# Performance work log

Measured on AMD Instinct MI355X. Metric: run time of the kernel, lower is better.

Reference implementation:

```python
import jax, jax.numpy as jnp
import numpy as np

N_AGENTS = 8
N_ENEMIES = 8
N_ALLIES = 7
H = 64            # rnn_hidden_dim (must be 64: Encoder latent dim hardcoded to 64, fed to fc3)
HEADS = 2         # hpn_head_num
OUT_NORMAL = 6    # output_normal_actions
N_ACTIONS = OUT_NORMAL + N_ENEMIES  # 14, required by expand_as in original code
E_DIM = 8
A_DIM = 8
OWN_DIM = 30
HYPER = 64        # hpn_hyper_dim
ENC_HID = 128     # predict_net_dim
BS = 2048


def _gru_cell(x, h, Wih, Whh, bih, bhh):
    # torch GRUCell math, gate order (r, z, n)
    gi = x @ Wih + bih
    gh = h @ Whh + bhh
    ir, iz, inn = jnp.split(gi, 3, axis=-1)
    hr, hz, hn = jnp.split(gh, 3, axis=-1)
    r = jax.nn.sigmoid(ir + hr)
    z = jax.nn.sigmoid(iz + hz)
    n = jnp.tanh(inn + r * hn)
    return (1.0 - z) * n + z * h


def setup_inputs() -> dict:
    key = jax.random.key(0)
    ks = jax.random.split(key, 48)
    B = BS * N_AGENTS

    def w(k, shape):
        return jax.random.normal(k, shape, dtype=jnp.float32) * 0.05

    he_out = ((E_DIM + 1) * H + 1) * HEADS   # 1154
    ha_out = A_DIM * H * HEADS               # 1024 (non-MMM map)

    return {
        "bs": BS,
        "own_feats": jax.random.normal(ks[0], (B, OWN_DIM), jnp.float32),
        "enemy_feats": jax.random.normal(ks[1], (B * N_ENEMIES, E_DIM), jnp.float32),
        "ally_feats": jax.random.normal(ks[2], (B * N_ALLIES, A_DIM), jnp.float32),
        "agent_ids": jax.random.randint(ks[3], (B,), 0, N_AGENTS),
        "last_action_ids": jax.random.randint(ks[4], (B,), 0, N_ACTIONS),
        "hidden_state": jax.random.normal(ks[5], (B, H), jnp.float32) * 0.1,
        "fc1_own_W": w(ks[6], (OWN_DIM, H)), "fc1_own_b": w(ks[7], (H,)),
        "agent_emb": w(ks[8], (N_AGENTS, H)),
        "action_emb": w(ks[9], (N_ACTIONS, H)),
        "he_W1": w(ks[10], (E_DIM, HYPER)), "he_b1": w(ks[11], (HYPER,)),
        "he_W2": w(ks[12], (HYPER, he_out)), "he_b2": w(ks[13], (he_out,)),
        "ha_W1": w(ks[14], (A_DIM, HYPER)), "ha_b1": w(ks[15], (HYPER,)),
        "ha_W2": w(ks[16], (HYPER, ha_out)), "ha_b2": w(ks[17], (ha_out,)),
        "merger_in_w": jnp.ones((1, HEADS, H), jnp.float32),
        "merger_out_w": jnp.ones((1, HEADS, 1), jnp.float32),
        "gru_Wih": w(ks[18], (H, 3 * H)), "gru_Whh": w(ks[19], (H, 3 * H)),
        "gru_bih": w(ks[20], (3 * H,)), "gru_bhh": w(ks[21], (3 * H,)),
        "fc2n_W": w(ks[22], (H, OUT_NORMAL)), "fc2n_b": w(ks[23], (OUT_NORMAL,)),
        "fc1b_W": w(ks[24], (OWN_DIM, H)), "fc1b_b": w(ks[25], (H,)),
        "gru2_Wih": w(ks[26], (H, 3 * H)), "gru2_Whh": w(ks[27], (H, 3 * H)),
        "gru2_bih": w(ks[28], (3 * H,)), "gru2_bhh": w(ks[29], (3 * H,)),
        "enc_W1": w(ks[30], (H, ENC_HID)), "enc_b1": w(ks[31], (ENC_HID,)),
        "enc_W2": w(ks[32], (ENC_HID, H)), "enc_b2": w(ks[33], (H,)),
        "fc3_W": w(ks[34], (H, N_ACTIONS)), "fc3_b": w(ks[35], (N_ACTIONS,)),
        "mlp_W": w(ks[36], (N_AGENTS, H, N_ACTIONS)), "mlp_b": w(ks[37], (N_AGENTS, N_ACTIONS)),
    }


def reference(bs, own_feats, enemy_feats, ally_feats, agent_ids, last_action_ids,
              hidden_state, fc1_own_W, fc1_own_b, agent_emb, action_emb,
              he_W1, he_b1, he_W2, he_b2, ha_W1, ha_b1, ha_W2, ha_b2,
              merger_in_w, merger_out_w, gru_Wih, gru_Whh, gru_bih, gru_bhh,
              fc2n_W, fc2n_b, fc1b_W, fc1b_b, gru2_Wih, gru2_Whh, gru2_bih, gru2_bhh,
              enc_W1, enc_b1, enc_W2, enc_b2, fc3_W, fc3_b, mlp_W, mlp_b):
    B = bs * N_AGENTS

    # own embedding + id/action embeddings
    emb_own = own_feats @ fc1_own_W + fc1_own_b
    emb_own = emb_own + agent_emb[agent_ids] + action_emb[last_action_ids]

    # hypernet-generated per-enemy fc1 weights, applied per entity, summed over enemies
    he = jax.nn.relu(enemy_feats @ he_W1 + he_b1) @ he_W2 + he_b2  # [B*E, 1154]
    cut = (H + 1) * HEADS
    w1e = he[:, :-cut].reshape(-1, E_DIM, H * HEADS)               # [B*E, e_dim, H*heads]
    emb_en = jnp.einsum('nd,ndk->nk', enemy_feats, w1e)
    emb_en = emb_en.reshape(B, N_ENEMIES, HEADS, H).sum(axis=1)    # [B, heads, H]

    ha = jax.nn.relu(ally_feats @ ha_W1 + ha_b1) @ ha_W2 + ha_b2   # [B*A, 1024]
    w1a = ha.reshape(-1, A_DIM, H * HEADS)
    emb_al = jnp.einsum('nd,ndk->nk', ally_feats, w1a)
    emb_al = emb_al.reshape(B, N_ALLIES, HEADS, H).sum(axis=1)     # [B, heads, H]

    # Merger over heads (softmax-weighted sum)
    mw = jax.nn.softmax(merger_in_w, axis=1)                       # [1, heads, H]
    merged = jnp.sum(mw * (emb_en + emb_al), axis=1)               # [B, H]

    x = jax.nn.relu(emb_own + merged)
    hh = _gru_cell(x, hidden_state, gru_Wih, gru_Whh, gru_bih, gru_bhh)  # [B, H]

    q_normal = (hh @ fc2n_W + fc2n_b).reshape(bs, N_AGENTS, OUT_NORMAL)

    # hypernet-generated attack output heads
    w2 = he[:, -cut:-HEADS].reshape(B, N_ENEMIES, H, HEADS)
    w2 = w2.transpose(0, 2, 1, 3).reshape(B, H, N_ENEMIES * HEADS)
    b2 = he[:, -HEADS:].reshape(B, N_ENEMIES * HEADS)
    qa = jnp.einsum('bh,bhk->bk', hh, w2) + b2                     # [B, E*heads]
    qa = qa.reshape(B * N_ENEMIES, HEADS)
    mo = jax.nn.softmax(merger_out_w[:, :, 0], axis=1)             # [1, heads]
    q_attack = jnp.sum(mo * qa, axis=1).reshape(bs, N_AGENTS, N_ENEMIES)

    q = jnp.concatenate([q_normal, q_attack], axis=-1)             # [bs, n_agents, 14]

    # parallel fc1 -> single-step GRU -> encoder branch
    x2 = jax.nn.relu(own_feats @ fc1b_W + fc1b_b)                  # [B, H]
    g = _gru_cell(x2, hidden_state, gru2_Wih, gru2_Whh, gru2_bih, gru2_bhh)  # [B, H]
    z = jax.nn.relu(g @ enc_W1 + enc_b1) @ enc_W2 + enc_b2         # [B, 64] encoder latent
    q_f = (z @ fc3_W + fc3_b).reshape(bs, N_AGENTS, N_ACTIONS)

    # per-agent mlps applied to first n_agents rows of gru output (as in original)
    ga = g[:N_AGENTS]                                              # [n_agents, H]
    local_q = jnp.einsum('ah,ahk->ak', ga, mlp_W) + mlp_b          # [n_agents, n_actions]
    local_qe = jnp.broadcast_to(local_q[None], q.shape)

    q_total = q + local_qe + q_f
    return (q_total, hh.reshape(bs, N_AGENTS, H), local_qe, q_f)
```

## Files before the change

kernel.cpp:

```cpp
#include <hip/hip_runtime.h>

#define HH_OFF 229376
#define LQE_OFF 1277952
#define QF_OFF 1507328

#define WS_HE 0
#define WS_HA 33280
#define WS_ATT 66560
#define WS_BATT 70656
#define WS_BH 70720
#define WS_BC 70784
#define WS_LQ 70800
#define WS_G1 70912
#define WS_G2 95488
#define WS_E1 120064
#define WS_E2 128256
#define WS_F1 136448
#define WS_END 140544

#define SSTR 640
#define BSTR 384

struct Params {
  const float *own, *ef, *af, *hid;
  const int *aid, *lid;
  const float *fc1oW, *fc1ob, *aemb, *actemb;
  const float *heW1, *heb1, *heW2, *heb2;
  const float *haW1, *hab1, *haW2, *hab2;
  const float *mi, *mo;
  const float *gWih, *gWhh, *gbih, *gbhh;
  const float *fc2nW, *fc2nb;
  const float *fc1bW, *fc1bb;
  const float *g2Wih, *g2Whh, *g2bih, *g2bhh;
  const float *eW1, *eb1, *eW2, *eb2;
  const float *fc3W, *fc3b;
  const float *mlpW, *mlpb;
};

__device__ __forceinline__ float sigm(float x) {
  x = fminf(fmaxf(x, -30.f), 30.f);
  return 1.f / (1.f + __expf(-x));
}
__device__ __forceinline__ float tanh_(float x) {
  x = fminf(fmaxf(x, -15.f), 15.f);
  float e = __expf(-2.f * x);
  return (1.f - e) / (1.f + e);
}

__global__ void __launch_bounds__(512) prep_kernel(Params p, float* __restrict__ ws) {
  const int tid = threadIdx.x;
  if (blockIdx.x == 0) {
    __shared__ float g8[8][64];
    __shared__ float x2s[8][64];
    const int w = __builtin_amdgcn_readfirstlane(tid >> 6);
    const int lane = tid & 63;
    {
      float acc = p.fc1bb[lane];
      const float* ow = p.own + w * 30;
      for (int d = 0; d < 30; ++d) acc += ow[d] * p.fc1bW[d * 64 + lane];
      x2s[w][lane] = fmaxf(acc, 0.f);
      float a0 = p.g2bih[lane], a1 = p.g2bih[64 + lane], a2 = p.g2bih[128 + lane];
      float b0 = p.g2bhh[lane], b1 = p.g2bhh[64 + lane], b2 = p.g2bhh[128 + lane];
      const float* hidw = p.hid + w * 64;
      for (int k = 0; k < 64; ++k) {
        float xk = x2s[w][k];
        float hk = hidw[k];
        a0 += xk * p.g2Wih[k * 192 + lane];
        a1 += xk * p.g2Wih[k * 192 + 64 + lane];
        a2 += xk * p.g2Wih[k * 192 + 128 + lane];
        b0 += hk * p.g2Whh[k * 192 + lane];
        b1 += hk * p.g2Whh[k * 192 + 64 + lane];
        b2 += hk * p.g2Whh[k * 192 + 128 + lane];
      }
      float r = sigm(a0 + b0), z = sigm(a1 + b1);
      float n = tanh_(a2 + r * b2);
      g8[w][lane] = (1.f - z) * n + z * hidw[lane];
    }
    __syncthreads();
    if (tid < 112) {
      int a = tid / 14, c = tid % 14;
      float lacc = p.mlpb[a * 14 + c];
      for (int h = 0; h < 64; ++h) lacc += g8[a][h] * p.mlpW[(a * 64 + h) * 14 + c];
      ws[WS_LQ + tid] = lacc;
    }
    return;
  }
  const int idx = (int)(blockIdx.x - 1) * 512 + tid;
  if (idx >= WS_END) return;
  const float mo0 = sigm(p.mo[0] - p.mo[1]);
  const float mo1 = 1.f - mo0;
  if (idx < 33280) {
    int c = idx >> 8, rem = idx & 255, h = rem >> 2, q = rem & 3;
    int t = c * 4 + q;
    float mw0 = sigm(p.mi[h] - p.mi[64 + h]);
    float mw1 = 1.f - mw0;
    float v;
    if (t < 512) {
      int d = t >> 6, j = t & 63;
      v = mw0 * p.heW2[j * 1154 + d * 128 + h] + mw1 * p.heW2[j * 1154 + d * 128 + 64 + h];
    } else {
      int d = t - 512;
      v = mw0 * p.heb2[d * 128 + h] + mw1 * p.heb2[d * 128 + 64 + h];
    }
    ws[WS_HE + idx] = v;
  } else if (idx < 66560) {
    int rel = idx - 33280;
    int c = rel >> 8, rem = rel & 255, h = rem >> 2, q = rem & 3;
    int t = c * 4 + q;
    float mw0 = sigm(p.mi[h] - p.mi[64 + h]);
    float mw1 = 1.f - mw0;
    float v;
    if (t < 512) {
      int d = t >> 6, j = t & 63;
      v = mw0 * p.haW2[j * 1024 + d * 128 + h] + mw1 * p.haW2[j * 1024 + d * 128 + 64 + h];
    } else {
      int d = t - 512;
      v = mw0 * p.hab2[d * 128 + h] + mw1 * p.hab2[d * 128 + 64 + h];
    }
    ws[WS_HA + rel] = v;
  } else if (idx < 70656) {
    int rel = idx - 66560;
    int c = rel >> 8, rem = rel & 255, j = rem >> 2, q = rem & 3;
    int h = c * 4 + q;
    ws[WS_ATT + rel] = mo0 * p.heW2[j * 1154 + 1024 + 2 * h] +
                       mo1 * p.heW2[j * 1154 + 1024 + 2 * h + 1];
  } else if (idx < 70720) {
    int j = idx - 70656;
    ws[WS_BATT + j] = mo0 * p.heW2[j * 1154 + 1152] + mo1 * p.heW2[j * 1154 + 1153];
  } else if (idx < 70784) {
    int h = idx - 70720;
    ws[WS_BH + h] = mo0 * p.heb2[1024 + 2 * h] + mo1 * p.heb2[1024 + 2 * h + 1];
  } else if (idx == 70784) {
    ws[WS_BC] = mo0 * p.heb2[1152] + mo1 * p.heb2[1153];
  } else if (idx < WS_G1) {
    return;
  } else if (idx < WS_G2) {
    int rel = idx - WS_G1;
    int k4 = rel / 1536, r2 = rel % 1536;
    int j = r2 >> 8, lane = (r2 & 255) >> 2, q = rel & 3;
    int row = 4 * k4 + q;
    ws[idx] = (j < 3) ? p.gWih[row * 192 + j * 64 + lane]
                      : p.gWhh[row * 192 + (j - 3) * 64 + lane];
  } else if (idx < WS_E1) {
    int rel = idx - WS_G2;
    int k4 = rel / 1536, r2 = rel % 1536;
    int j = r2 >> 8, lane = (r2 & 255) >> 2, q = rel & 3;
    int row = 4 * k4 + q;
    ws[idx] = (j < 3) ? p.g2Wih[row * 192 + j * 64 + lane]
                      : p.g2Whh[row * 192 + (j - 3) * 64 + lane];
  } else if (idx < WS_E2) {
    int rel = idx - WS_E1;
    int k4 = rel >> 9, j = (rel >> 8) & 1, lane = (rel & 255) >> 2, q = rel & 3;
    int row = 4 * k4 + q;
    ws[idx] = p.eW1[row * 128 + j * 64 + lane];
  } else if (idx < WS_F1) {
    int rel = idx - WS_E2;
    int k4 = rel >> 8, lane = (rel & 255) >> 2, q = rel & 3;
    int row = 4 * k4 + q;
    ws[idx] = p.eW2[row * 64 + lane];
  } else {
    int rel = idx - WS_F1;
    int k4 = rel >> 9, j = (rel >> 8) & 1, lane = (rel & 255) >> 2, q = rel & 3;
    int row = 4 * k4 + q;
    float v;
    if (row < 30) v = (j == 0) ? p.fc1oW[row * 64 + lane] : p.fc1bW[row * 64 + lane];
    else if (row == 30) v = (j == 0) ? p.fc1ob[lane] : p.fc1bb[lane];
    else v = 0.f;
    ws[idx] = v;
  }
}

__global__ void __launch_bounds__(256, 2) kernelA(Params p, const float* __restrict__ ws,
                                                  float* __restrict__ out) {
  __shared__ float smem[4 * 4 * SSTR];
  const int w = __builtin_amdgcn_readfirstlane((int)(threadIdx.x >> 6));
  const int lane = threadIdx.x & 63;
  float* S = &smem[w * 4 * SSTR];
  const int i0 = blockIdx.x * 16 + w * 4;

#pragma unroll
  for (int s = 0; s < 4; ++s) {
    S[s * SSTR + 520 + lane] = p.ef[(i0 + s) * 64 + lane];
    if (lane < 56) S[s * SSTR + 584 + lane] = p.af[(i0 + s) * 56 + lane];
  }
  float macc[4] = {0.f, 0.f, 0.f, 0.f};
  {
    float w1[8];
#pragma unroll
    for (int d = 0; d < 8; ++d) w1[d] = p.heW1[d * 64 + lane];
    const float b1 = p.heb1[lane];
#pragma unroll
    for (int s = 0; s < 4; ++s) {
      float T[8], fs[8];
#pragma unroll
      for (int d = 0; d < 8; ++d) { T[d] = 0.f; fs[d] = 0.f; }
#pragma unroll
      for (int e = 0; e < 8; ++e) {
        float4 a = *(const float4*)&S[s * SSTR + 520 + e * 8];
        float4 b = *(const float4*)&S[s * SSTR + 520 + e * 8 + 4];
        float acc = b1 + a.x * w1[0] + a.y * w1[1] + a.z * w1[2] + a.w * w1[3] +
                    b.x * w1[4] + b.y * w1[5] + b.z * w1[6] + b.w * w1[7];
        float r = fmaxf(acc, 0.f);
        T[0] += r * a.x; T[1] += r * a.y; T[2] += r * a.z; T[3] += r * a.w;
        T[4] += r * b.x; T[5] += r * b.y; T[6] += r * b.z; T[7] += r * b.w;
        fs[0] += a.x; fs[1] += a.y; fs[2] += a.z; fs[3] += a.w;
        fs[4] += b.x; fs[5] += b.y; fs[6] += b.z; fs[7] += b.w;
      }
#pragma unroll
      for (int d = 0; d < 8; ++d) S[s * SSTR + d * 64 + lane] = T[d];
      if (lane == 0) {
#pragma unroll
        for (int d = 0; d < 8; ++d) S[s * SSTR + 512 + d] = fs[d];
      }
    }
  }
  {
    const float4* W4 = (const float4*)(ws + WS_HE);
    for (int c = 0; c < 130; ++c) {
      float4 wv = W4[c * 64 + lane];
#pragma unroll
      for (int s = 0; s < 4; ++s) {
        float4 tv = *(const float4*)&S[s * SSTR + c * 4];
        macc[s] += tv.x * wv.x + tv.y * wv.y + tv.z * wv.z + tv.w * wv.w;
      }
    }
  }
  {
    float w1[8];
#pragma unroll
    for (int d = 0; d < 8; ++d) w1[d] = p.haW1[d * 64 + lane];
    const float b1 = p.hab1[lane];
#pragma unroll
    for (int s = 0; s < 4; ++s) {
      float T[8], fs[8];
#pragma unroll
      for (int d = 0; d < 8; ++d) { T[d] = 0.f; fs[d] = 0.f; }
#pragma unroll
      for (int e = 0; e < 7; ++e) {
        float4 a = *(const float4*)&S[s * SSTR + 584 + e * 8];
        float4 b = *(const float4*)&S[s * SSTR + 584 + e * 8 + 4];
        float acc = b1 + a.x * w1[0] + a.y * w1[1] + a.z * w1[2] + a.w * w1[3] +
                    b.x * w1[4] + b.y * w1[5] + b.z * w1[6] + b.w * w1[7];
        float r = fmaxf(acc, 0.f);
        T[0] += r * a.x; T[1] += r * a.y; T[2] += r * a.z; T[3] += r * a.w;
        T[4] += r * b.x; T[5] += r * b.y; T[6] += r * b.z; T[7] += r * b.w;
        fs[0] += a.x; fs[1] += a.y; fs[2] += a.z; fs[3] += a.w;
        fs[4] += b.x; fs[5] += b.y; fs[6] += b.z; fs[7] += b.w;
      }
#pragma unroll
      for (int d = 0; d < 8; ++d) S[s * SSTR + d * 64 + lane] = T[d];
      if (lane == 0) {
#pragma unroll
        for (int d = 0; d < 8; ++d) S[s * SSTR + 512 + d] = fs[d];
      }
    }
  }
  {
    const float4* W4 = (const float4*)(ws + WS_HA);
    for (int c = 0; c < 130; ++c) {
      float4 wv = W4[c * 64 + lane];
#pragma unroll
      for (int s = 0; s < 4; ++s) {
        float4 tv = *(const float4*)&S[s * SSTR + c * 4];
        macc[s] += tv.x * wv.x + tv.y * wv.y + tv.z * wv.z + tv.w * wv.w;
      }
    }
  }
#pragma unroll
  for (int s = 0; s < 4; ++s) {
    S[s * SSTR + 64 + lane] = p.hid[(i0 + s) * 64 + lane];
    if (lane < 32)
      S[s * SSTR + 584 + lane] =
          (lane < 30) ? p.own[(i0 + s) * 30 + lane] : (lane == 30 ? 1.f : 0.f);
  }
  {
    float aO[4] = {0.f, 0.f, 0.f, 0.f};
    const float4* F = (const float4*)(ws + WS_F1);
    for (int k4 = 0; k4 < 8; ++k4) {
      float4 wo = F[k4 * 128 + lane];
#pragma unroll
      for (int s = 0; s < 4; ++s) {
        float4 o4 = *(const float4*)&S[s * SSTR + 584 + k4 * 4];
        aO[s] += o4.x * wo.x + o4.y * wo.y + o4.z * wo.z + o4.w * wo.w;
      }
    }
#pragma unroll
    for (int s = 0; s < 4; ++s) {
      const int i = i0 + s;
      float x = aO[s] + p.aemb[p.aid[i] * 64 + lane] + p.actemb[p.lid[i] * 64 + lane] + macc[s];
      S[s * SSTR + lane] = fmaxf(x, 0.f);
    }
  }
  {
    const float bi0 = p.gbih[lane] + p.gbhh[lane];
    const float bi1 = p.gbih[64 + lane] + p.gbhh[64 + lane];
    const float bi2i = p.gbih[128 + lane];
    const float bi2h = p.gbhh[128 + lane];
    float A0[4], A1[4], A2[4], B2[4];
#pragma unroll
    for (int s = 0; s < 4; ++s) { A0[s] = bi0; A1[s] = bi1; A2[s] = bi2i; B2[s] = bi2h; }
    const float4* G = (const float4*)(ws + WS_G1);
    for (int k4 = 0; k4 < 16; ++k4) {
      float4 w0 = G[k4 * 384 + lane];
      float4 w1v = G[k4 * 384 + 64 + lane];
      float4 w2v = G[k4 * 384 + 128 + lane];
      float4 w3 = G[k4 * 384 + 192 + lane];
      float4 w4v = G[k4 * 384 + 256 + lane];
      float4 w5 = G[k4 * 384 + 320 + lane];
#pragma unroll
      for (int s = 0; s < 4; ++s) {
        float4 x4 = *(const float4*)&S[s * SSTR + k4 * 4];
        float4 h4 = *(const float4*)&S[s * SSTR + 64 + k4 * 4];
        A0[s] += x4.x * w0.x + x4.y * w0.y + x4.z * w0.z + x4.w * w0.w +
                 h4.x * w3.x + h4.y * w3.y + h4.z * w3.z + h4.w * w3.w;
        A1[s] += x4.x * w1v.x + x4.y * w1v.y + x4.z * w1v.z + x4.w * w1v.w +
                 h4.x * w4v.x + h4.y * w4v.y + h4.z * w4v.z + h4.w * w4v.w;
        A2[s] += x4.x * w2v.x + x4.y * w2v.y + x4.z * w2v.z + x4.w * w2v.w;
        B2[s] += h4.x * w5.x + h4.y * w5.y + h4.z * w5.z + h4.w * w5.w;
      }
    }
#pragma unroll
    for (int s = 0; s < 4; ++s) {
      float r = sigm(A0[s]);
      float z = sigm(A1[s]);
      float n = tanh_(A2[s] + r * B2[s]);
      float hp = S[s * SSTR + 64 + lane];
      float hh = (1.f - z) * n + z * hp;
      S[s * SSTR + 128 + lane] = hh;
      out[HH_OFF + (i0 + s) * 64 + lane] = hh;
    }
  }
  {
    float v4[4];
    const float batt = ws[WS_BATT + lane];
#pragma unroll
    for (int s = 0; s < 4; ++s) v4[s] = batt;
    const float4* A4 = (const float4*)(ws + WS_ATT);
    for (int c = 0; c < 16; ++c) {
      float4 wv = A4[c * 64 + lane];
#pragma unroll
      for (int s = 0; s < 4; ++s) {
        float4 h4 = *(const float4*)&S[s * SSTR + 128 + c * 4];
        v4[s] += h4.x * wv.x + h4.y * wv.y + h4.z * wv.z + h4.w * wv.w;
      }
    }
    float w1[8];
#pragma unroll
    for (int d = 0; d < 8; ++d) w1[d] = p.heW1[d * 64 + lane];
    const float b1 = p.heb1[lane];
    const float bhv = ws[WS_BH + lane];
    const float bc = ws[WS_BC];
#pragma unroll
    for (int s = 0; s < 4; ++s) {
      float red[9];
#pragma unroll
      for (int e = 0; e < 8; ++e) {
        float4 a = *(const float4*)&S[s * SSTR + 520 + e * 8];
        float4 b = *(const float4*)&S[s * SSTR + 520 + e * 8 + 4];
        float acc = b1 + a.x * w1[0] + a.y * w1[1] + a.z * w1[2] + a.w * w1[3] +
                    b.x * w1[4] + b.y * w1[5] + b.z * w1[6] + b.w * w1[7];
        red[e] = fmaxf(acc, 0.f) * v4[s];
      }
      red[8] = S[s * SSTR + 128 + lane] * bhv;
#pragma unroll
      for (int off = 32; off >= 1; off >>= 1) {
#pragma unroll
        for (int t = 0; t < 9; ++t) red[t] += __shfl_xor(red[t], off, 64);
      }
      if (lane == 0) {
#pragma unroll
        for (int e = 0; e < 8; ++e) S[s * SSTR + 448 + 6 + e] = red[e] + red[8] + bc;
      }
    }
  }
  if (lane < 56) {
    const int s = lane / 14, c = lane % 14;
    const int i = i0 + s;
    float qo;
    if (c < 6) {
      float acc = p.fc2nb[c];
      for (int h = 0; h < 64; ++h) acc += S[s * SSTR + 128 + h] * p.fc2nW[h * 6 + c];
      qo = acc;
    } else {
      qo = S[s * SSTR + 448 + c];
    }
    float lq = ws[WS_LQ + (i & 7) * 14 + c];
    out[i * 14 + c] = qo + lq;
    out[LQE_OFF + i * 14 + c] = lq;
  }
}

__global__ void __launch_bounds__(256, 2) kernelB(Params p, const float* __restrict__ ws,
                                                  float* __restrict__ out) {
  __shared__ float smem[4 * 4 * BSTR];
  const int w = __builtin_amdgcn_readfirstlane((int)(threadIdx.x >> 6));
  const int lane = threadIdx.x & 63;
  float* S = &smem[w * 4 * BSTR];
  const int i0 = blockIdx.x * 16 + w * 4;

#pragma unroll
  for (int s = 0; s < 4; ++s) {
    S[s * BSTR + 64 + lane] = p.hid[(i0 + s) * 64 + lane];
    if (lane < 32)
      S[s * BSTR + 192 + lane] =
          (lane < 30) ? p.own[(i0 + s) * 30 + lane] : (lane == 30 ? 1.f : 0.f);
  }
  {
    float aB[4] = {0.f, 0.f, 0.f, 0.f};
    const float4* F = (const float4*)(ws + WS_F1);
    for (int k4 = 0; k4 < 8; ++k4) {
      float4 wb = F[k4 * 128 + 64 + lane];
#pragma unroll
      for (int s = 0; s < 4; ++s) {
        float4 o4 = *(const float4*)&S[s * BSTR + 192 + k4 * 4];
        aB[s] += o4.x * wb.x + o4.y * wb.y + o4.z * wb.z + o4.w * wb.w;
      }
    }
#pragma unroll
    for (int s = 0; s < 4; ++s) S[s * BSTR + lane] = fmaxf(aB[s], 0.f);
  }
  {
    const float bi0 = p.g2bih[lane] + p.g2bhh[lane];
    const float bi1 = p.g2bih[64 + lane] + p.g2bhh[64 + lane];
    const float bi2i = p.g2bih[128 + lane];
    const float bi2h = p.g2bhh[128 + lane];
    float A0[4], A1[4], A2[4], B2[4];
#pragma unroll
    for (int s = 0; s < 4; ++s) { A0[s] = bi0; A1[s] = bi1; A2[s] = bi2i; B2[s] = bi2h; }
    const float4* G = (const float4*)(ws + WS_G2);
    for (int k4 = 0; k4 < 16; ++k4) {
      float4 w0 = G[k4 * 384 + lane];
      float4 w1v = G[k4 * 384 + 64 + lane];
      float4 w2v = G[k4 * 384 + 128 + lane];
      float4 w3 = G[k4 * 384 + 192 + lane];
      float4 w4v = G[k4 * 384 + 256 + lane];
      float4 w5 = G[k4 * 384 + 320 + lane];
#pragma unroll
      for (int s = 0; s < 4; ++s) {
        float4 x4 = *(const float4*)&S[s * BSTR + k4 * 4];
        float4 h4 = *(const float4*)&S[s * BSTR + 64 + k4 * 4];
        A0[s] += x4.x * w0.x + x4.y * w0.y + x4.z * w0.z + x4.w * w0.w +
                 h4.x * w3.x + h4.y * w3.y + h4.z * w3.z + h4.w * w3.w;
        A1[s] += x4.x * w1v.x + x4.y * w1v.y + x4.z * w1v.z + x4.w * w1v.w +
                 h4.x * w4v.x + h4.y * w4v.y + h4.z * w4v.z + h4.w * w4v.w;
        A2[s] += x4.x * w2v.x + x4.y * w2v.y + x4.z * w2v.z + x4.w * w2v.w;
        B2[s] += h4.x * w5.x + h4.y * w5.y + h4.z * w5.z + h4.w * w5.w;
      }
    }
#pragma unroll
    for (int s = 0; s < 4; ++s) {
      float r = sigm(A0[s]);
      float z = sigm(A1[s]);
      float n = tanh_(A2[s] + r * B2[s]);
      float hp = S[s * BSTR + 64 + lane];
      S[s * BSTR + 128 + lane] = (1.f - z) * n + z * hp;
    }
  }
  {
    float C0[4], C1[4];
#pragma unroll
    for (int s = 0; s < 4; ++s) { C0[s] = p.eb1[lane]; C1[s] = p.eb1[64 + lane]; }
    const float4* E1 = (const float4*)(ws + WS_E1);
    for (int k4 = 0; k4 < 16; ++k4) {
      float4 w0 = E1[k4 * 128 + lane];
      float4 w1v = E1[k4 * 128 + 64 + lane];
#pragma unroll
      for (int s = 0; s < 4; ++s) {
        float4 g4 = *(const float4*)&S[s * BSTR + 128 + k4 * 4];
        C0[s] += g4.x * w0.x + g4.y * w0.y + g4.z * w0.z + g4.w * w0.w;
        C1[s] += g4.x * w1v.x + g4.y * w1v.y + g4.z * w1v.z + g4.w * w1v.w;
      }
    }
#pragma unroll
    for (int s = 0; s < 4; ++s) {
      S[s * BSTR + 192 + lane] = fmaxf(C0[s], 0.f);
      S[s * BSTR + 256 + lane] = fmaxf(C1[s], 0.f);
    }
  }
  {
    float Z[4];
#pragma unroll
    for (int s = 0; s < 4; ++s) Z[s] = p.eb2[lane];
    const float4* E2 = (const float4*)(ws + WS_E2);
    for (int k4 = 0; k4 < 32; ++k4) {
      float4 wv = E2[k4 * 64 + lane];
#pragma unroll
      for (int s = 0; s < 4; ++s) {
        float4 z4 = *(const float4*)&S[s * BSTR + 192 + k4 * 4];
        Z[s] += z4.x * wv.x + z4.y * wv.y + z4.z * wv.z + z4.w * wv.w;
      }
    }
#pragma unroll
    for (int s = 0; s < 4; ++s) S[s * BSTR + 320 + lane] = Z[s];
  }
  if (lane < 56) {
    const int s = lane / 14, c = lane % 14;
    const int i = i0 + s;
    float qf = p.fc3b[c];
    for (int k = 0; k < 64; ++k) qf += S[s * BSTR + 320 + k] * p.fc3W[k * 14 + c];
    out[QF_OFF + i * 14 + c] = qf;
    out[i * 14 + c] += qf;
  }
}

extern "C" void kernel_launch(void* const* d_in, const int* in_sizes, int n_in,
                              void* d_out, int out_size, void* d_ws, size_t ws_size,
                              hipStream_t stream) {
  (void)in_sizes; (void)n_in; (void)out_size; (void)ws_size;
  Params p;
  p.own = (const float*)d_in[1];
  p.ef = (const float*)d_in[2];
  p.af = (const float*)d_in[3];
  p.aid = (const int*)d_in[4];
  p.lid = (const int*)d_in[5];
  p.hid = (const float*)d_in[6];
  p.fc1oW = (const float*)d_in[7];
  p.fc1ob = (const float*)d_in[8];
  p.aemb = (const float*)d_in[9];
  p.actemb = (const float*)d_in[10];
  p.heW1 = (const float*)d_in[11];
  p.heb1 = (const float*)d_in[12];
  p.heW2 = (const float*)d_in[13];
  p.heb2 = (const float*)d_in[14];
  p.haW1 = (const float*)d_in[15];
  p.hab1 = (const float*)d_in[16];
  p.haW2 = (const float*)d_in[17];
  p.hab2 = (const float*)d_in[18];
  p.mi = (const float*)d_in[19];
  p.mo = (const float*)d_in[20];
  p.gWih = (const float*)d_in[21];
  p.gWhh = (const float*)d_in[22];
  p.gbih = (const float*)d_in[23];
  p.gbhh = (const float*)d_in[24];
  p.fc2nW = (const float*)d_in[25];
  p.fc2nb = (const float*)d_in[26];
  p.fc1bW = (const float*)d_in[27];
  p.fc1bb = (const float*)d_in[28];
  p.g2Wih = (const float*)d_in[29];
  p.g2Whh = (const float*)d_in[30];
  p.g2bih = (const float*)d_in[31];
  p.g2bhh = (const float*)d_in[32];
  p.eW1 = (const float*)d_in[33];
  p.eb1 = (const float*)d_in[34];
  p.eW2 = (const float*)d_in[35];
  p.eb2 = (const float*)d_in[36];
  p.fc3W = (const float*)d_in[37];
  p.fc3b = (const float*)d_in[38];
  p.mlpW = (const float*)d_in[39];
  p.mlpb = (const float*)d_in[40];
  float* ws = (float*)d_ws;
  float* out = (float*)d_out;
  prep_kernel<<<dim3(276), dim3(512), 0, stream>>>(p, ws);
  kernelA<<<dim3(1024), dim3(256), 0, stream>>>(p, ws, out);
  kernelB<<<dim3(1024), dim3(256), 0, stream>>>(p, ws, out);
}
```

Before: 310.1 us.

## Use bf16 MFMA for hypernet weight contraction in kernelA

Replaces the scalar fp32 dot-product loops that contract the per-sample T vectors with the folded hyper-network weights (enemy and ally) by bf16 MFMA 16x16x32 instructions. The prep kernel now packs the folded weights into bf16 pairs laid out in MFMA fragment order, which halves workspace size. The T tensors are written to LDS as bf16, and the shared-memory layout is compacted to match. This trades fp32 precision for bf16 in a large reduction, which risks accuracy tolerance failures.

```diff
diff --git a/kernel.cpp b/kernel.cpp
--- a/kernel.cpp
+++ b/kernel.cpp
@@ -4,22 +4,27 @@
 #define LQE_OFF 1277952
 #define QF_OFF 1507328
 
-#define WS_HE 0
-#define WS_HA 33280
-#define WS_ATT 66560
-#define WS_BATT 70656
-#define WS_BH 70720
-#define WS_BC 70784
-#define WS_LQ 70800
-#define WS_G1 70912
-#define WS_G2 95488
-#define WS_E1 120064
-#define WS_E2 128256
-#define WS_F1 136448
-#define WS_END 140544
-
-#define SSTR 640
+#define WB_HE 0
+#define WB_HA 17408
+#define WS_ATT 34816
+#define WS_BATT 38912
+#define WS_BH 38976
+#define WS_BC 39040
+#define WS_LQ 39056
+#define WS_G1 39168
+#define WS_G2 63744
+#define WS_E1 88320
+#define WS_E2 96512
+#define WS_F1 104704
+#define WS_END 108800
+
+#define AWAVE 2448
+#define ASAMP 336
+#define TA_SH 552
 #define BSTR 384
+
+using s8v = __attribute__((ext_vector_type(8))) short;
+using f4v = __attribute__((ext_vector_type(4))) float;
 
 struct Params {
   const float *own, *ef, *af, *hid;
@@ -45,6 +50,33 @@
   x = fminf(fmaxf(x, -15.f), 15.f);
   float e = __expf(-2.f * x);
   return (1.f - e) / (1.f + e);
+}
+__device__ __forceinline__ unsigned short f2bf(float f) {
+  unsigned u = __float_as_uint(f);
+  return (unsigned short)((u + 0x7FFFu + ((u >> 16) & 1u)) >> 16);
+}
+
+__device__ __forceinline__ float hefold(const Params& p, int t, int h, float mw0, float mw1) {
+  if (t < 512) {
+    int d = t >> 6, j = t & 63;
+    return mw0 * p.heW2[j * 1154 + d * 128 + h] + mw1 * p.heW2[j * 1154 + d * 128 + 64 + h];
+  }
+  if (t < 520) {
+    int d = t - 512;
+    return mw0 * p.heb2[d * 128 + h] + mw1 * p.heb2[d * 128 + 64 + h];
+  }
+  return 0.f;
+}
+__device__ __forceinline__ float hafold(const Params& p, int t, int h, float mw0, float mw1) {
+  if (t < 512) {
+    int d = t >> 6, j = t & 63;
+    return mw0 * p.haW2[j * 1024 + d * 128 + h] + mw1 * p.haW2[j * 1024 + d * 128 + 64 + h];
+  }
+  if (t < 520) {
+    int d = t - 512;
+    return mw0 * p.hab2[d * 128 + h] + mw1 * p.hab2[d * 128 + 64 + h];
+  }
+  return 0.f;
 }
 
 __global__ void __launch_bounds__(512) prep_kernel(Params p, float* __restrict__ ws) {
@@ -89,49 +121,37 @@
   if (idx >= WS_END) return;
   const float mo0 = sigm(p.mo[0] - p.mo[1]);
   const float mo1 = 1.f - mo0;
-  if (idx < 33280) {
-    int c = idx >> 8, rem = idx & 255, h = rem >> 2, q = rem & 3;
-    int t = c * 4 + q;
+  if (idx < 34816) {
+    int rel = (idx < WB_HA) ? idx : idx - WB_HA;
+    int jp = rel & 3, lane = (rel >> 2) & 63, rest = rel >> 8;
+    int nc = rest & 3, ks = rest >> 2;
+    int t0 = ks * 32 + ((lane >> 4) << 3) + jp * 2;
+    int h = nc * 16 + (lane & 15);
     float mw0 = sigm(p.mi[h] - p.mi[64 + h]);
     float mw1 = 1.f - mw0;
-    float v;
-    if (t < 512) {
-      int d = t >> 6, j = t & 63;
-      v = mw0 * p.heW2[j * 1154 + d * 128 + h] + mw1 * p.heW2[j * 1154 + d * 128 + 64 + h];
+    float v0, v1;
+    if (idx < WB_HA) {
+      v0 = hefold(p, t0, h, mw0, mw1);
+      v1 = hefold(p, t0 + 1, h, mw0, mw1);
     } else {
-      int d = t - 512;
-      v = mw0 * p.heb2[d * 128 + h] + mw1 * p.heb2[d * 128 + 64 + h];
-    }
-    ws[WS_HE + idx] = v;
-  } else if (idx < 66560) {
-    int rel = idx - 33280;
-    int c = rel >> 8, rem = rel & 255, h = rem >> 2, q = rem & 3;
-    int t = c * 4 + q;
-    float mw0 = sigm(p.mi[h] - p.mi[64 + h]);
-    float mw1 = 1.f - mw0;
-    float v;
-    if (t < 512) {
-      int d = t >> 6, j = t & 63;
-      v = mw0 * p.haW2[j * 1024 + d * 128 + h] + mw1 * p.haW2[j * 1024 + d * 128 + 64 + h];
-    } else {
-      int d = t - 512;
-      v = mw0 * p.hab2[d * 128 + h] + mw1 * p.hab2[d * 128 + 64 + h];
-    }
-    ws[WS_HA + rel] = v;
-  } else if (idx < 70656) {
-    int rel = idx - 66560;
-    int c = rel >> 8, rem = rel & 255, j = rem >> 2, q = rem & 3;
+      v0 = hafold(p, t0, h, mw0, mw1);
+      v1 = hafold(p, t0 + 1, h, mw0, mw1);
+    }
+    unsigned pk = (unsigned)f2bf(v0) | ((unsigned)f2bf(v1) << 16);
+    ws[idx] = __uint_as_float(pk);
+  } else if (idx < 38912) {
+    int rel = idx - WS_ATT;
+    int c = rel >> 8, rem = rel & 255, j = rem >> 2, q = rel & 3;
     int h = c * 4 + q;
-    ws[WS_ATT + rel] = mo0 * p.heW2[j * 1154 + 1024 + 2 * h] +
-                       mo1 * p.heW2[j * 1154 + 1024 + 2 * h + 1];
-  } else if (idx < 70720) {
-    int j = idx - 70656;
-    ws[WS_BATT + j] = mo0 * p.heW2[j * 1154 + 1152] + mo1 * p.heW2[j * 1154 + 1153];
-  } else if (idx < 70784) {
-    int h = idx - 70720;
-    ws[WS_BH + h] = mo0 * p.heb2[1024 + 2 * h] + mo1 * p.heb2[1024 + 2 * h + 1];
-  } else if (idx == 70784) {
-    ws[WS_BC] = mo0 * p.heb2[1152] + mo1 * p.heb2[1153];
+    ws[idx] = mo0 * p.heW2[j * 1154 + 1024 + 2 * h] + mo1 * p.heW2[j * 1154 + 1024 + 2 * h + 1];
+  } else if (idx < 38976) {
+    int j = idx - WS_BATT;
+    ws[idx] = mo0 * p.heW2[j * 1154 + 1152] + mo1 * p.heW2[j * 1154 + 1153];
+  } else if (idx < 39040) {
+    int h = idx - WS_BH;
+    ws[idx] = mo0 * p.heb2[1024 + 2 * h] + mo1 * p.heb2[1024 + 2 * h + 1];
+  } else if (idx == WS_BC) {
+    ws[idx] = mo0 * p.heb2[1152] + mo1 * p.heb2[1153];
   } else if (idx < WS_G1) {
     return;
   } else if (idx < WS_G2) {
@@ -172,18 +192,23 @@
 
 __global__ void __launch_bounds__(256, 2) kernelA(Params p, const float* __restrict__ ws,
                                                   float* __restrict__ out) {
-  __shared__ float smem[4 * 4 * SSTR];
+  __shared__ float smem[4 * AWAVE];
   const int w = __builtin_amdgcn_readfirstlane((int)(threadIdx.x >> 6));
   const int lane = threadIdx.x & 63;
-  float* S = &smem[w * 4 * SSTR];
+  float* S = &smem[w * AWAVE];
+  unsigned short* ta = (unsigned short*)S;
+  float* SB = S + 1104;
   const int i0 = blockIdx.x * 16 + w * 4;
 
+  if (lane < 24) {
+#pragma unroll
+    for (int m = 0; m < 4; ++m) ta[m * TA_SH + 520 + lane] = 0;
+  }
 #pragma unroll
   for (int s = 0; s < 4; ++s) {
-    S[s * SSTR + 520 + lane] = p.ef[(i0 + s) * 64 + lane];
-    if (lane < 56) S[s * SSTR + 584 + lane] = p.af[(i0 + s) * 56 + lane];
-  }
-  float macc[4] = {0.f, 0.f, 0.f, 0.f};
+    SB[s * ASAMP + 208 + lane] = p.ef[(i0 + s) * 64 + lane];
+    if (lane < 56) SB[s * ASAMP + 272 + lane] = p.af[(i0 + s) * 56 + lane];
+  }
   {
     float w1[8];
 #pragma unroll
@@ -196,8 +221,8 @@
       for (int d = 0; d < 8; ++d) { T[d] = 0.f; fs[d] = 0.f; }
 #pragma unroll
       for (int e = 0; e < 8; ++e) {
-        float4 a = *(const float4*)&S[s * SSTR + 520 + e * 8];
-        float4 b = *(const float4*)&S[s * SSTR + 520 + e * 8 + 4];
+        float4 a = *(const float4*)&SB[s * ASAMP + 208 + e * 8];
+        float4 b = *(const float4*)&SB[s * ASAMP + 208 + e * 8 + 4];
         float acc = b1 + a.x * w1[0] + a.y * w1[1] + a.z * w1[2] + a.w * w1[3] +
                     b.x * w1[4] + b.y * w1[5] + b.z * w1[6] + b.w * w1[7];
         float r = fmaxf(acc, 0.f);
@@ -207,21 +232,24 @@
         fs[4] += b.x; fs[5] += b.y; fs[6] += b.z; fs[7] += b.w;
       }
 #pragma unroll
-      for (int d = 0; d < 8; ++d) S[s * SSTR + d * 64 + lane] = T[d];
+      for (int d = 0; d < 8; ++d) ta[s * TA_SH + d * 64 + lane] = f2bf(T[d]);
       if (lane == 0) {
 #pragma unroll
-        for (int d = 0; d < 8; ++d) S[s * SSTR + 512 + d] = fs[d];
-      }
-    }
-  }
-  {
-    const float4* W4 = (const float4*)(ws + WS_HE);
-    for (int c = 0; c < 130; ++c) {
-      float4 wv = W4[c * 64 + lane];
-#pragma unroll
-      for (int s = 0; s < 4; ++s) {
-        float4 tv = *(const float4*)&S[s * SSTR + c * 4];
-        macc[s] += tv.x * wv.x + tv.y * wv.y + tv.z * wv.z + tv.w * wv.w;
+        for (int d = 0; d < 8; ++d) ta[s * TA_SH + 512 + d] = f2bf(fs[d]);
+      }
+    }
+  }
+  f4v acc[4];
+#pragma unroll
+  for (int nc = 0; nc < 4; ++nc) acc[nc] = (f4v){0.f, 0.f, 0.f, 0.f};
+  {
+    const s8v* WB = (const s8v*)(ws + WB_HE);
+    for (int ks = 0; ks < 17; ++ks) {
+      s8v a = *(const s8v*)&ta[(lane & 3) * TA_SH + ks * 32 + ((lane >> 4) << 3)];
+#pragma unroll
+      for (int nc = 0; nc < 4; ++nc) {
+        s8v b = WB[(ks * 4 + nc) * 64 + lane];
+        acc[nc] = __builtin_amdgcn_mfma_f32_16x16x32_bf16(a, b, acc[nc], 0, 0, 0);
       }
     }
   }
@@ -237,40 +265,47 @@
       for (int d = 0; d < 8; ++d) { T[d] = 0.f; fs[d] = 0.f; }
 #pragma unroll
       for (int e = 0; e < 7; ++e) {
-        float4 a = *(const float4*)&S[s * SSTR + 584 + e * 8];
-        float4 b = *(const float4*)&S[s * SSTR + 584 + e * 8 + 4];
-        float acc = b1 + a.x * w1[0] + a.y * w1[1] + a.z * w1[2] + a.w * w1[3] +
-                    b.x * w1[4] + b.y * w1[5] + b.z * w1[6] + b.w * w1[7];
-        float r = fmaxf(acc, 0.f);
+        float4 a = *(const float4*)&SB[s * ASAMP + 272 + e * 8];
+        float4 b = *(const float4*)&SB[s * ASAMP + 272 + e * 8 + 4];
+        float acc2 = b1 + a.x * w1[0] + a.y * w1[1] + a.z * w1[2] + a.w * w1[3] +
+                     b.x * w1[4] + b.y * w1[5] + b.z * w1[6] + b.w * w1[7];
+        float r = fmaxf(acc2, 0.f);
         T[0] += r * a.x; T[1] += r * a.y; T[2] += r * a.z; T[3] += r * a.w;
         T[4] += r * b.x; T[5] += r * b.y; T[6] += r * b.z; T[7] += r * b.w;
         fs[0] += a.x; fs[1] += a.y; fs[2] += a.z; fs[3] += a.w;
         fs[4] += b.x; fs[5] += b.y; fs[6] += b.z; fs[7] += b.w;
       }
 #pragma unroll
-      for (int d = 0; d < 8; ++d) S[s * SSTR + d * 64 + lane] = T[d];
+      for (int d = 0; d < 8; ++d) ta[s * TA_SH + d * 64 + lane] = f2bf(T[d]);
       if (lane == 0) {
 #pragma unroll
-        for (int d = 0; d < 8; ++d) S[s * SSTR + 512 + d] = fs[d];
-      }
-    }
-  }
-  {
-    const float4* W4 = (const float4*)(ws + WS_HA);
-    for (int c = 0; c < 130; ++c) {
-      float4 wv = W4[c * 64 + lane];
-#pragma unroll
-      for (int s = 0; s < 4; ++s) {
-        float4 tv = *(const float4*)&S[s * SSTR + c * 4];
-        macc[s] += tv.x * wv.x + tv.y * wv.y + tv.z * wv.z + tv.w * wv.w;
-      }
+        for (int d = 0; d < 8; ++d) ta[s * TA_SH + 512 + d] = f2bf(fs[d]);
+      }
+    }
+  }
+  {
+    const s8v* WB = (const s8v*)(ws + WB_HA);
+    for (int ks = 0; ks < 17; ++ks) {
+      s8v a = *(const s8v*)&ta[(lane & 3) * TA_SH + ks * 32 + ((lane >> 4) << 3)];
+#pragma unroll
+      for (int nc = 0; nc < 4; ++nc) {
+        s8v b = WB[(ks * 4 + nc) * 64 + lane];
+        acc[nc] = __builtin_amdgcn_mfma_f32_16x16x32_bf16(a, b, acc[nc], 0, 0, 0);
+      }
+    }
+  }
+  if (lane < 16) {
+#pragma unroll
+    for (int nc = 0; nc < 4; ++nc) {
+#pragma unroll
+      for (int r = 0; r < 4; ++r) SB[r * ASAMP + nc * 16 + lane] = acc[nc][r];
     }
   }
 #pragma unroll
   for (int s = 0; s < 4; ++s) {
-    S[s * SSTR + 64 + lane] = p.hid[(i0 + s) * 64 + lane];
+    SB[s * ASAMP + 64 + lane] = p.hid[(i0 + s) * 64 + lane];
     if (lane < 32)
-      S[s * SSTR + 584 + lane] =
+      SB[s * ASAMP + 272 + lane] =
           (lane < 30) ? p.own[(i0 + s) * 30 + lane] : (lane == 30 ? 1.f : 0.f);
   }
   {
@@ -280,15 +315,16 @@
       float4 wo = F[k4 * 128 + lane];
 #pragma unroll
       for (int s = 0; s < 4; ++s) {
-        float4 o4 = *(const float4*)&S[s * SSTR + 584 + k4 * 4];
+        float4 o4 = *(const float4*)&SB[s * ASAMP + 272 + k4 * 4];
         aO[s] += o4.x * wo.x + o4.y * wo.y + o4.z * wo.z + o4.w * wo.w;
       }
     }
 #pragma unroll
     for (int s = 0; s < 4; ++s) {
       const int i = i0 + s;
-      float x = aO[s] + p.aemb[p.aid[i] * 64 + lane] + p.actemb[p.lid[i] * 64 + lane] + macc[s];
-      S[s * SSTR + lane] = fmaxf(x, 0.f);
+      float mer = SB[s * ASAMP + lane];
+      float x = aO[s] + p.aemb[p.aid[i] * 64 + lane] + p.actemb[p.lid[i] * 64 + lane] + mer;
+      SB[s * ASAMP + lane] = fmaxf(x, 0.f);
     }
   }
   {
@@ -309,8 +345,8 @@
       float4 w5 = G[k4 * 384 + 320 + lane];
 #pragma unroll
       for (int s = 0; s < 4; ++s) {
-        float4 x4 = *(const float4*)&S[s * SSTR + k4 * 4];
-        float4 h4 = *(const float4*)&S[s * SSTR + 64 + k4 * 4];
+        float4 x4 = *(const float4*)&SB[s * ASAMP + k4 * 4];
+        float4 h4 = *(const float4*)&SB[s * ASAMP + 64 + k4 * 4];
         A0[s] += x4.x * w0.x + x4.y * w0.y + x4.z * w0.z + x4.w * w0.w +
                  h4.x * w3.x + h4.y * w3.y + h4.z * w3.z + h4.w * w3.w;
         A1[s] += x4.x * w1v.x + x4.y * w1v.y + x4.z * w1v.z + x4.w * w1v.w +
@@ -324,9 +360,9 @@
       float r = sigm(A0[s]);
       float z = sigm(A1[s]);
       float n = tanh_(A2[s] + r * B2[s]);
-      float hp = S[s * SSTR + 64 + lane];
+      float hp = SB[s * ASAMP + 64 + lane];
       float hh = (1.f - z) * n + z * hp;
-      S[s * SSTR + 128 + lane] = hh;
+      SB[s * ASAMP + 128 + lane] = hh;
       out[HH_OFF + (i0 + s) * 64 + lane] = hh;
     }
   }
@@ -340,7 +376,7 @@
       float4 wv = A4[c * 64 + lane];
 #pragma unroll
       for (int s = 0; s < 4; ++s) {
-        float4 h4 = *(const float4*)&S[s * SSTR + 128 + c * 4];
+        float4 h4 = *(const float4*)&SB[s * ASAMP + 128 + c * 4];
         v4[s] += h4.x * wv.x + h4.y * wv.y + h4.z * wv.z + h4.w * wv.w;
       }
     }
@@ -355,13 +391,13 @@
       float red[9];
 #pragma unroll
       for (int e = 0; e < 8; ++e) {
-        float4 a = *(const float4*)&S[s * SSTR + 520 + e * 8];
-        float4 b = *(const float4*)&S[s * SSTR + 520 + e * 8 + 4];
-        float acc = b1 + a.x * w1[0] + a.y * w1[1] + a.z * w1[2] + a.w * w1[3] +
-                    b.x * w1[4] + b.y * w1[5] + b.z * w1[6] + b.w * w1[7];
-        red[e] = fmaxf(acc, 0.f) * v4[s];
-      }
-      red[8] = S[s * SSTR + 128 + lane] * bhv;
+        float4 a = *(const float4*)&SB[s * ASAMP + 208 + e * 8];
+        float4 b = *(const float4*)&SB[s * ASAMP + 208 + e * 8 + 4];
+        float acc2 = b1 + a.x * w1[0] + a.y * w1[1] + a.z * w1[2] + a.w * w1[3] +
+                     b.x * w1[4] + b.y * w1[5] + b.z * w1[6] + b.w * w1[7];
+        red[e] = fmaxf(acc2, 0.f) * v4[s];
+      }
+      red[8] = SB[s * ASAMP + 128 + lane] * bhv;
 #pragma unroll
       for (int off = 32; off >= 1; off >>= 1) {
 #pragma unroll
@@ -369,7 +405,7 @@
       }
       if (lane == 0) {
 #pragma unroll
-        for (int e = 0; e < 8; ++e) S[s * SSTR + 448 + 6 + e] = red[e] + red[8] + bc;
+        for (int e = 0; e < 8; ++e) SB[s * ASAMP + 192 + 6 + e] = red[e] + red[8] + bc;
       }
     }
   }
@@ -378,11 +414,11 @@
     const int i = i0 + s;
     float qo;
     if (c < 6) {
-      float acc = p.fc2nb[c];
-      for (int h = 0; h < 64; ++h) acc += S[s * SSTR + 128 + h] * p.fc2nW[h * 6 + c];
-      qo = acc;
+      float a2 = p.fc2nb[c];
+      for (int h = 0; h < 64; ++h) a2 += SB[s * ASAMP + 128 + h] * p.fc2nW[h * 6 + c];
+      qo = a2;
     } else {
-      qo = S[s * SSTR + 448 + c];
+      qo = SB[s * ASAMP + 192 + c];
     }
     float lq = ws[WS_LQ + (i & 7) * 14 + c];
     out[i * 14 + c] = qo + lq;
@@ -550,7 +586,7 @@
   p.mlpb = (const float*)d_in[40];
   float* ws = (float*)d_ws;
   float* out = (float*)d_out;
-  prep_kernel<<<dim3(276), dim3(512), 0, stream>>>(p, ws);
+  prep_kernel<<<dim3(214), dim3(512), 0, stream>>>(p, ws);
   kernelA<<<dim3(1024), dim3(256), 0, stream>>>(p, ws, out);
   kernelB<<<dim3(1024), dim3(256), 0, stream>>>(p, ws, out);
 }
```

New measurement: 272.4 us. 12.2% less time.
